# Kernel optimization log

Hardware: AMD Instinct MI355X
Metric: run time of the kernel (lower is better)

## Reference

```python
import jax, jax.numpy as jnp
import numpy as np

N, D, H, C, E, K = 32768, 1024, 512, 512, 8, 2

def setup_inputs() -> dict:
    key = jax.random.key(0)
    ks = jax.random.split(key, 7)
    s = lambda fan_in: 1.0 / np.sqrt(fan_in)
    return {
        "x":  jax.random.normal(ks[0], (N, D), dtype=jnp.float32),
        "W1": jax.random.uniform(ks[1], (E, D, H), minval=-s(D), maxval=s(D), dtype=jnp.float32),
        "b1": jax.random.uniform(ks[2], (E, H), minval=-s(D), maxval=s(D), dtype=jnp.float32),
        "W2": jax.random.uniform(ks[3], (E, H, C), minval=-s(H), maxval=s(H), dtype=jnp.float32),
        "b2": jax.random.uniform(ks[4], (E, C), minval=-s(H), maxval=s(H), dtype=jnp.float32),
        "Wg": jax.random.uniform(ks[5], (D, E), minval=-s(D), maxval=s(D), dtype=jnp.float32),
        "bg": jax.random.uniform(ks[6], (E,), minval=-s(D), maxval=s(D), dtype=jnp.float32),
    }

def reference(x, W1, b1, W2, b2, Wg, bg):
    # Gating: dense gate vector with softmax(top-k logits) scattered into top-k slots
    gate_logits = x @ Wg + bg                               # [N, E]
    top_vals, top_idx = jax.lax.top_k(gate_logits, K)       # [N, K]
    gate = jnp.zeros_like(gate_logits).at[
        jnp.arange(x.shape[0])[:, None], top_idx
    ].set(jax.nn.softmax(top_vals, axis=-1))                # [N, E]
    # Dense all-experts FFN (as in the original module; dropout inactive at eval)
    h = jax.nn.relu(jnp.einsum('nd,edh->enh', x, W1) + b1[:, None, :])   # [E, N, H]
    out = jnp.einsum('enh,ehc->enc', h, W2) + b2[:, None, :]             # [E, N, C]
    # Masked weighted combine
    return jnp.einsum('ne,enc->nc', gate, out)              # [N, C]
```

## Files before the change

### kernel.cpp

```cpp
#include <hip/hip_runtime.h>

#define NTOK 32768
#define DDIM 1024
#define HDIM 512
#define CDIM 512
#define NEXP 8

#define BM 128
#define BN 128
#define BK 64
#define PITCH 72
#define MAXTILE 520

typedef __attribute__((ext_vector_type(8))) __bf16 bf16x8;
typedef __attribute__((ext_vector_type(4))) float f32x4;
typedef __attribute__((ext_vector_type(4))) unsigned short us4;
typedef __attribute__((ext_vector_type(8))) unsigned short us8;

static __device__ __forceinline__ unsigned short f2bf(float f) {
  union { float f; unsigned u; } v; v.f = f;
  unsigned u = v.u;
  u += 0x7FFFu + ((u >> 16) & 1u);
  return (unsigned short)(u >> 16);
}

static __device__ __forceinline__ float bf2f(unsigned short s) {
  union { unsigned u; float f; } v;
  v.u = ((unsigned)s) << 16;
  return v.f;
}

__global__ __launch_bounds__(256) void transpose_bf16_kernel(
    const float* __restrict__ in, unsigned short* __restrict__ out,
    int R, int Cc) {
  __shared__ float tile[32][33];
  int e = blockIdx.z;
  int c0 = blockIdx.x * 32, r0 = blockIdx.y * 32;
  const float* src = in + (size_t)e * R * Cc;
  unsigned short* dst = out + (size_t)e * R * Cc;
  int tx = threadIdx.x, ty = threadIdx.y;
#pragma unroll
  for (int i = 0; i < 32; i += 8)
    tile[ty + i][tx] = src[(size_t)(r0 + ty + i) * Cc + (c0 + tx)];
  __syncthreads();
#pragma unroll
  for (int i = 0; i < 32; i += 8)
    dst[(size_t)(c0 + ty + i) * R + (r0 + tx)] = f2bf(tile[tx][ty + i]);
}

#define GWPITCH 1064
#define XSLOT 1056

__global__ __launch_bounds__(256) void gate_kernel(
    const float* __restrict__ x, const float* __restrict__ Wg,
    const float* __restrict__ bg, int* __restrict__ sel,
    float* __restrict__ wpair, unsigned short* __restrict__ xb) {
  __shared__ float wg_lds[NEXP * GWPITCH];
  __shared__ float xs[4][XSLOT];

  int t = threadIdx.x;
  for (int i = t; i < DDIM * NEXP / 4; i += 256) {
    f32x4 v = *(const f32x4*)(Wg + (size_t)i * 4);
    int d = i >> 1;
    int e0 = (i & 1) * 4;
    int dsk = d + 4 * (d >> 7);
#pragma unroll
    for (int z = 0; z < 4; ++z)
      wg_lds[(e0 + z) * GWPITCH + dsk] = v[z];
  }
  __syncthreads();

  int wave = t >> 6, lane = t & 63;
  int g = lane >> 3, e = lane & 7;
  float* xslab = xs[wave];
  const float* wgrow = wg_lds + e * GWPITCH + g * 132;
  const float* xsg = xslab + g * 132;
  double bge = (double)bg[e];

  int n0 = blockIdx.x * 32 + wave * 8;
  f32x4 ld[4], ldn[4];
  {
    const f32x4* xrow = (const f32x4*)(x + (size_t)n0 * DDIM);
#pragma unroll
    for (int j = 0; j < 4; ++j) ld[j] = xrow[j * 64 + lane];
  }

#pragma unroll 1
  for (int r = 0; r < 8; ++r) {
    int n = n0 + r;
    unsigned short* xbr = xb + (size_t)n * DDIM;
#pragma unroll
    for (int j = 0; j < 4; ++j) {
      int d0 = j * 256 + lane * 4;
      *(f32x4*)&xslab[d0 + 4 * (d0 >> 7)] = ld[j];
      us4 o;
#pragma unroll
      for (int z = 0; z < 4; ++z) o[z] = f2bf(ld[j][z]);
      *(us4*)&xbr[d0] = o;
    }
    if (r < 7) {
      const f32x4* xr2 = (const f32x4*)(x + (size_t)(n + 1) * DDIM);
#pragma unroll
      for (int j = 0; j < 4; ++j) ldn[j] = xr2[j * 64 + lane];
    }
    float s0 = 0.0f, c0 = 0.0f, s1 = 0.0f, c1 = 0.0f;
#pragma unroll
    for (int k = 0; k < 32; ++k) {
      f32x4 xv = *(const f32x4*)&xsg[4 * k];
      f32x4 wv = *(const f32x4*)&wgrow[4 * k];
#pragma unroll
      for (int z = 0; z < 4; z += 2) {
        float p0 = xv[z] * wv[z];
        float y0 = p0 - c0;
        float t0 = s0 + y0;
        c0 = (t0 - s0) - y0;
        s0 = t0;
        float p1 = xv[z + 1] * wv[z + 1];
        float y1 = p1 - c1;
        float t1 = s1 + y1;
        c1 = (t1 - s1) - y1;
        s1 = t1;
      }
    }
    double p = ((double)s0 + (double)c0) + ((double)s1 + (double)c1);
    p += __shfl_xor(p, 8, 64);
    p += __shfl_xor(p, 16, 64);
    p += __shfl_xor(p, 32, 64);
    double mylg = p + bge;
    double lg[NEXP];
#pragma unroll
    for (int ee = 0; ee < NEXP; ++ee) lg[ee] = __shfl(mylg, ee, 64);
    if (lane == 0) {
      int e0i = 0;
#pragma unroll
      for (int ee = 1; ee < NEXP; ++ee) if (lg[ee] > lg[e0i]) e0i = ee;
      int e1i = (e0i == 0) ? 1 : 0;
#pragma unroll
      for (int ee = 0; ee < NEXP; ++ee)
        if (ee != e0i && lg[ee] > lg[e1i]) e1i = ee;
      float w1 = 1.0f / (1.0f + expf((float)(lg[e0i] - lg[e1i])));
      float w0 = 1.0f - w1;
      sel[n] = e0i | (e1i << 4);
      wpair[n * 2] = w0;
      wpair[n * 2 + 1] = w1;
    }
#pragma unroll
    for (int j = 0; j < 4; ++j) ld[j] = ldn[j];
  }
}

__global__ __launch_bounds__(1024) void build_lists_kernel(
    const int* __restrict__ sel, int* __restrict__ counts,
    int* __restrict__ lists) {
  int e = blockIdx.x;
  int t = threadIdx.x;
  __shared__ int sc[1024];
  int base = t * (NTOK / 1024);
  int cnt = 0;
#pragma unroll
  for (int i = 0; i < NTOK / 1024; ++i) {
    int s = sel[base + i];
    cnt += ((s & 15) == e) || (((s >> 4) & 15) == e);
  }
  sc[t] = cnt;
  __syncthreads();
  for (int d = 1; d < 1024; d <<= 1) {
    int v = (t >= d) ? sc[t - d] : 0;
    __syncthreads();
    sc[t] += v;
    __syncthreads();
  }
  int off = sc[t] - cnt;
#pragma unroll
  for (int i = 0; i < NTOK / 1024; ++i) {
    int s = sel[base + i];
    if ((s & 15) == e)
      lists[e * NTOK + off++] = (base + i) * 2;
    else if (((s >> 4) & 15) == e)
      lists[e * NTOK + off++] = (base + i) * 2 + 1;
  }
  if (t == 1023) counts[e] = sc[1023];
}

__global__ __launch_bounds__(256) void make_tiles_kernel(
    const int* __restrict__ counts, int* __restrict__ tiles) {
  __shared__ int off[NEXP + 1];
  int t = threadIdx.x;
  if (t == 0) {
    int s = 0;
    for (int e = 0; e < NEXP; ++e) { off[e] = s; s += (counts[e] + BM - 1) / BM; }
    off[NEXP] = s;
    tiles[0] = s;
  }
  __syncthreads();
  for (int e = 0; e < NEXP; ++e) {
    int base = off[e], cnt = off[e + 1] - off[e];
    for (int k = t; k < cnt; k += 256) {
      tiles[1 + 2 * (base + k)] = e;
      tiles[2 + 2 * (base + k)] = k * BM;
    }
  }
}

static __device__ __forceinline__ bool decode_tile(
    const int* tiles, const int* counts, int& e, int& ne, int& row0, int& col0) {
  int i = blockIdx.x;
  int xcd = i & 7, slot = i >> 3;
  int col = slot & 3, tslot = slot >> 2;
  int rt = tslot * 8 + xcd;
  if (rt >= tiles[0]) return false;
  e = tiles[1 + 2 * rt];
  row0 = tiles[2 + 2 * rt];
  ne = counts[e];
  col0 = col * BN;
  return true;
}

__global__ __launch_bounds__(256) void gemm1_kernel(
    const unsigned short* __restrict__ xb, const unsigned short* __restrict__ W1t,
    const float* __restrict__ b1, const int* __restrict__ lists,
    const int* __restrict__ counts, const int* __restrict__ tiles,
    unsigned short* __restrict__ h) {
  int e, ne, row0, col0;
  if (!decode_tile(tiles, counts, e, ne, row0, col0)) return;

  __shared__ unsigned short sA[BM * PITCH];
  __shared__ unsigned short sB[BN * PITCH];
  __shared__ int sTok[BM];

  int t = threadIdx.x;
  if (t < BM) {
    int r = row0 + t;
    sTok[t] = (r < ne) ? lists[e * NTOK + r] : -1;
  }
  __syncthreads();

  int arow = t >> 3, akq = t & 7;
  const unsigned short* aSrc[4];
  const unsigned short* bSrc[4];
  int wOff[4];
#pragma unroll
  for (int j = 0; j < 4; ++j) {
    int p = sTok[j * 32 + arow];
    int tok = (p < 0) ? 0 : (p >> 1);
    aSrc[j] = xb + (size_t)tok * DDIM + akq * 8;
    int c = col0 + j * 32 + arow;
    bSrc[j] = W1t + ((size_t)e * HDIM + c) * DDIM + akq * 8;
    wOff[j] = (j * 32 + arow) * PITCH + akq * 8;
  }

  int wave = t >> 6, lane = t & 63;
  int wr = wave >> 1, wc = wave & 1;
  int aBase = (wr * 64 + (lane & 15)) * PITCH + (lane >> 4) * 8;
  int bBase = (wc * 64 + (lane & 15)) * PITCH + (lane >> 4) * 8;

  f32x4 acc[4][4];
#pragma unroll
  for (int m = 0; m < 4; ++m)
#pragma unroll
    for (int nn = 0; nn < 4; ++nn) acc[m][nn] = (f32x4)0.0f;

  us8 aReg[4], bReg[4];
#pragma unroll
  for (int j = 0; j < 4; ++j) aReg[j] = *(const us8*)(aSrc[j]);
#pragma unroll
  for (int j = 0; j < 4; ++j) bReg[j] = *(const us8*)(bSrc[j]);
#pragma unroll
  for (int j = 0; j < 4; ++j) *(us8*)&sA[wOff[j]] = aReg[j];
#pragma unroll
  for (int j = 0; j < 4; ++j) *(us8*)&sB[wOff[j]] = bReg[j];
  __syncthreads();

  const int NKT = DDIM / BK;
  for (int kt = 0; kt < NKT; ++kt) {
    if (kt + 1 < NKT) {
#pragma unroll
      for (int j = 0; j < 4; ++j) aReg[j] = *(const us8*)(aSrc[j] + (kt + 1) * BK);
#pragma unroll
      for (int j = 0; j < 4; ++j) bReg[j] = *(const us8*)(bSrc[j] + (kt + 1) * BK);
    }
#pragma unroll
    for (int ks = 0; ks < 2; ++ks) {
      bf16x8 af[4], bfr[4];
#pragma unroll
      for (int m = 0; m < 4; ++m)
        af[m] = *(const bf16x8*)&sA[aBase + m * 16 * PITCH + ks * 32];
#pragma unroll
      for (int nn = 0; nn < 4; ++nn)
        bfr[nn] = *(const bf16x8*)&sB[bBase + nn * 16 * PITCH + ks * 32];
#pragma unroll
      for (int m = 0; m < 4; ++m)
#pragma unroll
        for (int nn = 0; nn < 4; ++nn)
          acc[m][nn] = __builtin_amdgcn_mfma_f32_16x16x32_bf16(
              af[m], bfr[nn], acc[m][nn], 0, 0, 0);
    }
    __syncthreads();
    if (kt + 1 < NKT) {
#pragma unroll
      for (int j = 0; j < 4; ++j) *(us8*)&sA[wOff[j]] = aReg[j];
#pragma unroll
      for (int j = 0; j < 4; ++j) *(us8*)&sB[wOff[j]] = bReg[j];
    }
    __syncthreads();
  }

  int cBase = col0 + wc * 64 + (lane & 15);
  float b1c[4];
#pragma unroll
  for (int nn = 0; nn < 4; ++nn) b1c[nn] = b1[e * HDIM + cBase + nn * 16];
#pragma unroll
  for (int m = 0; m < 4; ++m) {
#pragma unroll
    for (int q = 0; q < 4; ++q) {
      int rloc = wr * 64 + m * 16 + (lane >> 4) * 4 + q;
      if (row0 + rloc < ne) {
        int p = sTok[rloc];
        unsigned short* hr = h + (size_t)p * HDIM;
#pragma unroll
        for (int nn = 0; nn < 4; ++nn) {
          float v = acc[m][nn][q] + b1c[nn];
          v = fmaxf(v, 0.0f);
          hr[cBase + nn * 16] = f2bf(v);
        }
      }
    }
  }
}

__global__ __launch_bounds__(256) void gemm2_kernel(
    const unsigned short* __restrict__ h, const unsigned short* __restrict__ W2t,
    const float* __restrict__ b2, const int* __restrict__ lists,
    const int* __restrict__ counts, const int* __restrict__ tiles,
    unsigned short* __restrict__ obuf) {
  int e, ne, row0, col0;
  if (!decode_tile(tiles, counts, e, ne, row0, col0)) return;

  __shared__ unsigned short sA[BM * PITCH];
  __shared__ unsigned short sB[BN * PITCH];
  __shared__ int sTok[BM];

  int t = threadIdx.x;
  if (t < BM) {
    int r = row0 + t;
    sTok[t] = (r < ne) ? lists[e * NTOK + r] : -1;
  }
  __syncthreads();

  int arow = t >> 3, akq = t & 7;
  const unsigned short* aSrc[4];
  const unsigned short* bSrc[4];
  int wOff[4];
#pragma unroll
  for (int j = 0; j < 4; ++j) {
    int p = sTok[j * 32 + arow];
    int pp = (p < 0) ? 0 : p;
    aSrc[j] = h + (size_t)pp * HDIM + akq * 8;
    int c = col0 + j * 32 + arow;
    bSrc[j] = W2t + ((size_t)e * CDIM + c) * HDIM + akq * 8;
    wOff[j] = (j * 32 + arow) * PITCH + akq * 8;
  }

  int wave = t >> 6, lane = t & 63;
  int wr = wave >> 1, wc = wave & 1;
  int aBase = (wr * 64 + (lane & 15)) * PITCH + (lane >> 4) * 8;
  int bBase = (wc * 64 + (lane & 15)) * PITCH + (lane >> 4) * 8;

  f32x4 acc[4][4];
#pragma unroll
  for (int m = 0; m < 4; ++m)
#pragma unroll
    for (int nn = 0; nn < 4; ++nn) acc[m][nn] = (f32x4)0.0f;

  us8 aReg[4], bReg[4];
#pragma unroll
  for (int j = 0; j < 4; ++j) aReg[j] = *(const us8*)(aSrc[j]);
#pragma unroll
  for (int j = 0; j < 4; ++j) bReg[j] = *(const us8*)(bSrc[j]);
#pragma unroll
  for (int j = 0; j < 4; ++j) *(us8*)&sA[wOff[j]] = aReg[j];
#pragma unroll
  for (int j = 0; j < 4; ++j) *(us8*)&sB[wOff[j]] = bReg[j];
  __syncthreads();

  const int NKT = HDIM / BK;
  for (int kt = 0; kt < NKT; ++kt) {
    if (kt + 1 < NKT) {
#pragma unroll
      for (int j = 0; j < 4; ++j) aReg[j] = *(const us8*)(aSrc[j] + (kt + 1) * BK);
#pragma unroll
      for (int j = 0; j < 4; ++j) bReg[j] = *(const us8*)(bSrc[j] + (kt + 1) * BK);
    }
#pragma unroll
    for (int ks = 0; ks < 2; ++ks) {
      bf16x8 af[4], bfr[4];
#pragma unroll
      for (int m = 0; m < 4; ++m)
        af[m] = *(const bf16x8*)&sA[aBase + m * 16 * PITCH + ks * 32];
#pragma unroll
      for (int nn = 0; nn < 4; ++nn)
        bfr[nn] = *(const bf16x8*)&sB[bBase + nn * 16 * PITCH + ks * 32];
#pragma unroll
      for (int m = 0; m < 4; ++m)
#pragma unroll
        for (int nn = 0; nn < 4; ++nn)
          acc[m][nn] = __builtin_amdgcn_mfma_f32_16x16x32_bf16(
              af[m], bfr[nn], acc[m][nn], 0, 0, 0);
    }
    __syncthreads();
    if (kt + 1 < NKT) {
#pragma unroll
      for (int j = 0; j < 4; ++j) *(us8*)&sA[wOff[j]] = aReg[j];
#pragma unroll
      for (int j = 0; j < 4; ++j) *(us8*)&sB[wOff[j]] = bReg[j];
    }
    __syncthreads();
  }

  int cBase = col0 + wc * 64 + (lane & 15);
  float b2c[4];
#pragma unroll
  for (int nn = 0; nn < 4; ++nn) b2c[nn] = b2[e * CDIM + cBase + nn * 16];
#pragma unroll
  for (int m = 0; m < 4; ++m) {
#pragma unroll
    for (int q = 0; q < 4; ++q) {
      int rloc = wr * 64 + m * 16 + (lane >> 4) * 4 + q;
      if (row0 + rloc < ne) {
        int p = sTok[rloc];
        unsigned short* orow = obuf + (size_t)p * CDIM;
#pragma unroll
        for (int nn = 0; nn < 4; ++nn)
          orow[cBase + nn * 16] = f2bf(acc[m][nn][q] + b2c[nn]);
      }
    }
  }
}

__global__ __launch_bounds__(256) void combine_kernel(
    const float* __restrict__ wpair, float* __restrict__ out) {
  const unsigned short* obuf = (const unsigned short*)out;
  int t = threadIdx.x;
  int n = blockIdx.x * 4 + (t >> 6);
  int c = (t & 63) * 8;
  us8 a = *(const us8*)&obuf[(size_t)(2 * n) * CDIM + c];
  us8 b = *(const us8*)&obuf[(size_t)(2 * n + 1) * CDIM + c];
  float w0 = wpair[2 * n], w1 = wpair[2 * n + 1];
  f32x4 r0, r1;
#pragma unroll
  for (int z = 0; z < 4; ++z) {
    r0[z] = w0 * bf2f(a[z]) + w1 * bf2f(b[z]);
    r1[z] = w0 * bf2f(a[z + 4]) + w1 * bf2f(b[z + 4]);
  }
  __syncthreads();
  *(f32x4*)&out[(size_t)n * CDIM + c] = r0;
  *(f32x4*)&out[(size_t)n * CDIM + c + 4] = r1;
}

extern "C" void kernel_launch(void* const* d_in, const int* in_sizes, int n_in,
                              void* d_out, int out_size, void* d_ws, size_t ws_size,
                              hipStream_t stream) {
  const float* x  = (const float*)d_in[0];
  const float* W1 = (const float*)d_in[1];
  const float* b1 = (const float*)d_in[2];
  const float* W2 = (const float*)d_in[3];
  const float* b2 = (const float*)d_in[4];
  const float* Wg = (const float*)d_in[5];
  const float* bg = (const float*)d_in[6];
  float* out = (float*)d_out;
  char* ws = (char*)d_ws;

  int* counts = (int*)ws;
  float* wpair = (float*)(ws + 256);
  int* sel = (int*)(ws + 256 + 262144);
  int* lists = (int*)(ws + 256 + 262144 + 131072);
  int* tiles = (int*)(ws + 256 + 262144 + 131072 + 1048576);
  unsigned short* W1t = (unsigned short*)(ws + 256 + 262144 + 131072 + 1048576 + 8192);
  unsigned short* W2t = W1t + (size_t)NEXP * HDIM * DDIM;
  unsigned short* hbuf = W2t + (size_t)NEXP * CDIM * HDIM;

  unsigned short* xb = (unsigned short*)d_out;
  unsigned short* obuf = (unsigned short*)d_out;

  hipLaunchKernelGGL(transpose_bf16_kernel, dim3(HDIM / 32, DDIM / 32, NEXP),
                     dim3(32, 8), 0, stream, W1, W1t, DDIM, HDIM);
  hipLaunchKernelGGL(transpose_bf16_kernel, dim3(CDIM / 32, HDIM / 32, NEXP),
                     dim3(32, 8), 0, stream, W2, W2t, HDIM, CDIM);
  hipLaunchKernelGGL(gate_kernel, dim3(NTOK / 32), dim3(256), 0, stream,
                     x, Wg, bg, sel, wpair, xb);
  hipLaunchKernelGGL(build_lists_kernel, dim3(NEXP), dim3(1024), 0, stream,
                     sel, counts, lists);
  hipLaunchKernelGGL(make_tiles_kernel, dim3(1), dim3(256), 0, stream,
                     counts, tiles);
  hipLaunchKernelGGL(gemm1_kernel, dim3((MAXTILE / 8) * 4 * 8), dim3(256),
                     0, stream, xb, W1t, b1, lists, counts, tiles, hbuf);
  hipLaunchKernelGGL(gemm2_kernel, dim3((MAXTILE / 8) * 4 * 8), dim3(256),
                     0, stream, hbuf, W2t, b2, lists, counts, tiles, obuf);
  hipLaunchKernelGGL(combine_kernel, dim3(NTOK / 4), dim3(256), 0, stream,
                     wpair, out);
}
```

Before: 297.0 us.

## Load GEMM tiles directly into LDS with XOR-swizzled layout

Both expert GEMM kernels now use global_load_lds to copy A and B tiles straight from global memory into shared memory, with no staging in registers. The padded pitch is replaced by an XOR swizzle on 16-byte slots to avoid LDS bank conflicts. The register-prefetch software pipeline is removed, so each k-step waits for its own DMA before computing. This cuts VGPR use and LDS write instructions but loses the overlap of global loads with MFMA work inside a block.

```diff
diff --git a/kernel.cpp b/kernel.cpp
--- a/kernel.cpp
+++ b/kernel.cpp
@@ -9,7 +9,6 @@
 #define BM 128
 #define BN 128
 #define BK 64
-#define PITCH 72
 #define MAXTILE 520
 
 typedef __attribute__((ext_vector_type(8))) __bf16 bf16x8;
@@ -28,6 +27,27 @@
   union { unsigned u; float f; } v;
   v.u = ((unsigned)s) << 16;
   return v.f;
+}
+
+static __device__ __forceinline__ void gl_lds16(const void* g, void* l) {
+  __builtin_amdgcn_global_load_lds(
+      (const __attribute__((address_space(1))) unsigned int*)(unsigned long long)g,
+      (__attribute__((address_space(3))) unsigned int*)(unsigned)(unsigned long long)l,
+      16, 0, 0);
+}
+
+static __device__ __forceinline__ void fence_dma_then_barrier() {
+  __builtin_amdgcn_sched_barrier(0);
+  asm volatile("s_waitcnt vmcnt(0)" ::: "memory");
+  __builtin_amdgcn_sched_barrier(0);
+  __syncthreads();
+}
+
+static __device__ __forceinline__ void fence_lds_then_barrier() {
+  __builtin_amdgcn_sched_barrier(0);
+  asm volatile("s_waitcnt lgkmcnt(0)" ::: "memory");
+  __builtin_amdgcn_sched_barrier(0);
+  __syncthreads();
 }
 
 __global__ __launch_bounds__(256) void transpose_bf16_kernel(
@@ -224,8 +244,8 @@
   int e, ne, row0, col0;
   if (!decode_tile(tiles, counts, e, ne, row0, col0)) return;
 
-  __shared__ unsigned short sA[BM * PITCH];
-  __shared__ unsigned short sB[BN * PITCH];
+  __shared__ __attribute__((aligned(128))) unsigned short sA[BM * BK];
+  __shared__ __attribute__((aligned(128))) unsigned short sB[BN * BK];
   __shared__ int sTok[BM];
 
   int t = threadIdx.x;
@@ -235,59 +255,52 @@
   }
   __syncthreads();
 
-  int arow = t >> 3, akq = t & 7;
+  int srow = t >> 3;
+  int sslot = (t & 7) ^ (srow & 7);
   const unsigned short* aSrc[4];
   const unsigned short* bSrc[4];
-  int wOff[4];
+  unsigned short* aDst[4];
+  unsigned short* bDst[4];
+  int wbase = (t >> 6) * 512;
 #pragma unroll
   for (int j = 0; j < 4; ++j) {
-    int p = sTok[j * 32 + arow];
+    int p = sTok[j * 32 + srow];
     int tok = (p < 0) ? 0 : (p >> 1);
-    aSrc[j] = xb + (size_t)tok * DDIM + akq * 8;
-    int c = col0 + j * 32 + arow;
-    bSrc[j] = W1t + ((size_t)e * HDIM + c) * DDIM + akq * 8;
-    wOff[j] = (j * 32 + arow) * PITCH + akq * 8;
+    aSrc[j] = xb + (size_t)tok * DDIM + sslot * 8;
+    int c = col0 + j * 32 + srow;
+    bSrc[j] = W1t + ((size_t)e * HDIM + c) * DDIM + sslot * 8;
+    aDst[j] = &sA[j * 2048 + wbase];
+    bDst[j] = &sB[j * 2048 + wbase];
   }
 
   int wave = t >> 6, lane = t & 63;
   int wr = wave >> 1, wc = wave & 1;
-  int aBase = (wr * 64 + (lane & 15)) * PITCH + (lane >> 4) * 8;
-  int bBase = (wc * 64 + (lane & 15)) * PITCH + (lane >> 4) * 8;
+  int fr = lane & 15, fg = lane >> 4;
 
   f32x4 acc[4][4];
 #pragma unroll
   for (int m = 0; m < 4; ++m)
 #pragma unroll
     for (int nn = 0; nn < 4; ++nn) acc[m][nn] = (f32x4)0.0f;
-
-  us8 aReg[4], bReg[4];
-#pragma unroll
-  for (int j = 0; j < 4; ++j) aReg[j] = *(const us8*)(aSrc[j]);
-#pragma unroll
-  for (int j = 0; j < 4; ++j) bReg[j] = *(const us8*)(bSrc[j]);
-#pragma unroll
-  for (int j = 0; j < 4; ++j) *(us8*)&sA[wOff[j]] = aReg[j];
-#pragma unroll
-  for (int j = 0; j < 4; ++j) *(us8*)&sB[wOff[j]] = bReg[j];
-  __syncthreads();
 
   const int NKT = DDIM / BK;
   for (int kt = 0; kt < NKT; ++kt) {
-    if (kt + 1 < NKT) {
-#pragma unroll
-      for (int j = 0; j < 4; ++j) aReg[j] = *(const us8*)(aSrc[j] + (kt + 1) * BK);
-#pragma unroll
-      for (int j = 0; j < 4; ++j) bReg[j] = *(const us8*)(bSrc[j] + (kt + 1) * BK);
-    }
+#pragma unroll
+    for (int j = 0; j < 4; ++j) {
+      gl_lds16(aSrc[j] + kt * BK, aDst[j]);
+      gl_lds16(bSrc[j] + kt * BK, bDst[j]);
+    }
+    fence_dma_then_barrier();
 #pragma unroll
     for (int ks = 0; ks < 2; ++ks) {
+      int sl = (fg + ks * 4) ^ (fr & 7);
       bf16x8 af[4], bfr[4];
 #pragma unroll
       for (int m = 0; m < 4; ++m)
-        af[m] = *(const bf16x8*)&sA[aBase + m * 16 * PITCH + ks * 32];
+        af[m] = *(const bf16x8*)&sA[(wr * 64 + m * 16 + fr) * 64 + sl * 8];
 #pragma unroll
       for (int nn = 0; nn < 4; ++nn)
-        bfr[nn] = *(const bf16x8*)&sB[bBase + nn * 16 * PITCH + ks * 32];
+        bfr[nn] = *(const bf16x8*)&sB[(wc * 64 + nn * 16 + fr) * 64 + sl * 8];
 #pragma unroll
       for (int m = 0; m < 4; ++m)
 #pragma unroll
@@ -295,17 +308,10 @@
           acc[m][nn] = __builtin_amdgcn_mfma_f32_16x16x32_bf16(
               af[m], bfr[nn], acc[m][nn], 0, 0, 0);
     }
-    __syncthreads();
-    if (kt + 1 < NKT) {
-#pragma unroll
-      for (int j = 0; j < 4; ++j) *(us8*)&sA[wOff[j]] = aReg[j];
-#pragma unroll
-      for (int j = 0; j < 4; ++j) *(us8*)&sB[wOff[j]] = bReg[j];
-    }
-    __syncthreads();
-  }
-
-  int cBase = col0 + wc * 64 + (lane & 15);
+    fence_lds_then_barrier();
+  }
+
+  int cBase = col0 + wc * 64 + fr;
   float b1c[4];
 #pragma unroll
   for (int nn = 0; nn < 4; ++nn) b1c[nn] = b1[e * HDIM + cBase + nn * 16];
@@ -313,7 +319,7 @@
   for (int m = 0; m < 4; ++m) {
 #pragma unroll
     for (int q = 0; q < 4; ++q) {
-      int rloc = wr * 64 + m * 16 + (lane >> 4) * 4 + q;
+      int rloc = wr * 64 + m * 16 + fg * 4 + q;
       if (row0 + rloc < ne) {
         int p = sTok[rloc];
         unsigned short* hr = h + (size_t)p * HDIM;
@@ -336,8 +342,8 @@
   int e, ne, row0, col0;
   if (!decode_tile(tiles, counts, e, ne, row0, col0)) return;
 
-  __shared__ unsigned short sA[BM * PITCH];
-  __shared__ unsigned short sB[BN * PITCH];
+  __shared__ __attribute__((aligned(128))) unsigned short sA[BM * BK];
+  __shared__ __attribute__((aligned(128))) unsigned short sB[BN * BK];
   __shared__ int sTok[BM];
 
   int t = threadIdx.x;
@@ -347,59 +353,52 @@
   }
   __syncthreads();
 
-  int arow = t >> 3, akq = t & 7;
+  int srow = t >> 3;
+  int sslot = (t & 7) ^ (srow & 7);
   const unsigned short* aSrc[4];
   const unsigned short* bSrc[4];
-  int wOff[4];
+  unsigned short* aDst[4];
+  unsigned short* bDst[4];
+  int wbase = (t >> 6) * 512;
 #pragma unroll
   for (int j = 0; j < 4; ++j) {
-    int p = sTok[j * 32 + arow];
+    int p = sTok[j * 32 + srow];
     int pp = (p < 0) ? 0 : p;
-    aSrc[j] = h + (size_t)pp * HDIM + akq * 8;
-    int c = col0 + j * 32 + arow;
-    bSrc[j] = W2t + ((size_t)e * CDIM + c) * HDIM + akq * 8;
-    wOff[j] = (j * 32 + arow) * PITCH + akq * 8;
+    aSrc[j] = h + (size_t)pp * HDIM + sslot * 8;
+    int c = col0 + j * 32 + srow;
+    bSrc[j] = W2t + ((size_t)e * CDIM + c) * HDIM + sslot * 8;
+    aDst[j] = &sA[j * 2048 + wbase];
+    bDst[j] = &sB[j * 2048 + wbase];
   }
 
   int wave = t >> 6, lane = t & 63;
   int wr = wave >> 1, wc = wave & 1;
-  int aBase = (wr * 64 + (lane & 15)) * PITCH + (lane >> 4) * 8;
-  int bBase = (wc * 64 + (lane & 15)) * PITCH + (lane >> 4) * 8;
+  int fr = lane & 15, fg = lane >> 4;
 
   f32x4 acc[4][4];
 #pragma unroll
   for (int m = 0; m < 4; ++m)
 #pragma unroll
     for (int nn = 0; nn < 4; ++nn) acc[m][nn] = (f32x4)0.0f;
-
-  us8 aReg[4], bReg[4];
-#pragma unroll
-  for (int j = 0; j < 4; ++j) aReg[j] = *(const us8*)(aSrc[j]);
-#pragma unroll
-  for (int j = 0; j < 4; ++j) bReg[j] = *(const us8*)(bSrc[j]);
-#pragma unroll
-  for (int j = 0; j < 4; ++j) *(us8*)&sA[wOff[j]] = aReg[j];
-#pragma unroll
-  for (int j = 0; j < 4; ++j) *(us8*)&sB[wOff[j]] = bReg[j];
-  __syncthreads();
 
   const int NKT = HDIM / BK;
   for (int kt = 0; kt < NKT; ++kt) {
-    if (kt + 1 < NKT) {
-#pragma unroll
-      for (int j = 0; j < 4; ++j) aReg[j] = *(const us8*)(aSrc[j] + (kt + 1) * BK);
-#pragma unroll
-      for (int j = 0; j < 4; ++j) bReg[j] = *(const us8*)(bSrc[j] + (kt + 1) * BK);
-    }
+#pragma unroll
+    for (int j = 0; j < 4; ++j) {
+      gl_lds16(aSrc[j] + kt * BK, aDst[j]);
+      gl_lds16(bSrc[j] + kt * BK, bDst[j]);
+    }
+    fence_dma_then_barrier();
 #pragma unroll
     for (int ks = 0; ks < 2; ++ks) {
+      int sl = (fg + ks * 4) ^ (fr & 7);
       bf16x8 af[4], bfr[4];
 #pragma unroll
       for (int m = 0; m < 4; ++m)
-        af[m] = *(const bf16x8*)&sA[aBase + m * 16 * PITCH + ks * 32];
+        af[m] = *(const bf16x8*)&sA[(wr * 64 + m * 16 + fr) * 64 + sl * 8];
 #pragma unroll
       for (int nn = 0; nn < 4; ++nn)
-        bfr[nn] = *(const bf16x8*)&sB[bBase + nn * 16 * PITCH + ks * 32];
+        bfr[nn] = *(const bf16x8*)&sB[(wc * 64 + nn * 16 + fr) * 64 + sl * 8];
 #pragma unroll
       for (int m = 0; m < 4; ++m)
 #pragma unroll
@@ -407,17 +406,10 @@
           acc[m][nn] = __builtin_amdgcn_mfma_f32_16x16x32_bf16(
               af[m], bfr[nn], acc[m][nn], 0, 0, 0);
     }
-    __syncthreads();
-    if (kt + 1 < NKT) {
-#pragma unroll
-      for (int j = 0; j < 4; ++j) *(us8*)&sA[wOff[j]] = aReg[j];
-#pragma unroll
-      for (int j = 0; j < 4; ++j) *(us8*)&sB[wOff[j]] = bReg[j];
-    }
-    __syncthreads();
-  }
-
-  int cBase = col0 + wc * 64 + (lane & 15);
+    fence_lds_then_barrier();
+  }
+
+  int cBase = col0 + wc * 64 + fr;
   float b2c[4];
 #pragma unroll
   for (int nn = 0; nn < 4; ++nn) b2c[nn] = b2[e * CDIM + cBase + nn * 16];
@@ -425,7 +417,7 @@
   for (int m = 0; m < 4; ++m) {
 #pragma unroll
     for (int q = 0; q < 4; ++q) {
-      int rloc = wr * 64 + m * 16 + (lane >> 4) * 4 + q;
+      int rloc = wr * 64 + m * 16 + fg * 4 + q;
       if (row0 + rloc < ne) {
         int p = sTok[rloc];
         unsigned short* orow = obuf + (size_t)p * CDIM;
```

After: 248.5 us (median of 3 runs). -16.3%, faster.
